# Optimization experiments

Hardware: AMD Instinct MI355X
Metric: run time of the kernel (lower is better)

Reference implementation:

```python
import jax, jax.numpy as jnp
import numpy as np

EPS = 1e-8


def setup_inputs() -> dict:
    key = jax.random.key(0)
    k1, k2, k3 = jax.random.split(key, 3)
    B, N, K, D = 64, 4096, 64, 256
    x = jax.random.normal(k1, (B, N, D), dtype=jnp.float32)
    mu = jax.random.normal(k2, (K, D), dtype=jnp.float32)
    log_sigma = jax.random.normal(k3, (K, D), dtype=jnp.float32) * 0.1
    return {"x": x, "mu": mu, "log_sigma": log_sigma, "n_slots": 8}


def reference(x, mu, log_sigma, n_slots):
    # cosine similarity: normalize then contract (avoids [B,N,K,D] broadcast)
    xn = x / jnp.maximum(jnp.linalg.norm(x, axis=-1, keepdims=True), EPS)
    mn = mu / jnp.maximum(jnp.linalg.norm(mu, axis=-1, keepdims=True), EPS)
    cos = jnp.einsum('bnd,kd->bnk', xn, mn)            # [B, N, K]
    cos_soft = jax.nn.softmax(cos, axis=-1)            # softmax over concepts
    r = jax.nn.softmax(cos_soft.sum(axis=1), axis=-1)  # [B, K]
    _, idx = jax.lax.top_k(r, n_slots)                 # [B, n_slots]
    mu_sample = mu[idx]                                # [B, n_slots, D]
    sigma_sample = jnp.exp(log_sigma[idx])             # [B, n_slots, D]
    noise = jax.random.normal(jax.random.key(42), mu_sample.shape, dtype=mu_sample.dtype)
    return mu_sample + sigma_sample * noise
```

## Files before the change

### kernel.cpp

```cpp
#include <hip/hip_runtime.h>
#include <math.h>
#include <stdint.h>

#define B_ 64
#define N_ 4096
#define K_ 64
#define D_ 256
#define NS_ 8
#define XPAD 260

#define FENCE_LGKM() asm volatile("s_waitcnt lgkmcnt(0)" ::: "memory")
#define CBAR() asm volatile("" ::: "memory")

__device__ __forceinline__ float fadd(float a, float b) { return __fadd_rn(a, b); }
__device__ __forceinline__ float fmul(float a, float b) { return __fmul_rn(a, b); }

__device__ __forceinline__ float np_expf(float x) {
  const float LOG2E = 1.442695040888963407359924681001892137f;
  float qf = rintf(__fmul_rn(x, LOG2E));
  float r = __fmaf_rn(qf, -6.93145752e-1f, x);
  r = __fmaf_rn(qf, -1.42860677e-6f, r);
  float num = __fmaf_rn(r, 5.082762527590693718096e-04f, 6.757896990527504603057e-03f);
  num = __fmaf_rn(num, r, 5.114512081637298353406e-02f);
  num = __fmaf_rn(num, r, 2.473615434895520810817e-01f);
  num = __fmaf_rn(num, r, 7.257664613233124478488e-01f);
  num = __fmaf_rn(num, r, 9.999999999980870924916e-01f);
  float den = __fmaf_rn(r, 2.159509375685829852307e-02f, -2.742335390411667452936e-01f);
  den = __fmaf_rn(den, r, 1.000000000000000000000e+00f);
  float poly = __fdiv_rn(num, den);
  int qi = (int)qf;
  float scale = __int_as_float((127 + qi) << 23);
  return __fmul_rn(poly, scale);
}

__device__ __forceinline__ uint32_t rotl32(uint32_t x, int r) {
  return (x << r) | (x >> (32 - r));
}
__device__ __forceinline__ float jax_normal_from_index(uint32_t i) {
  uint32_t x0 = 0u, x1 = i;
  const uint32_t ks0 = 0u, ks1 = 42u, ks2 = 0x1BD11BDAu ^ 0u ^ 42u;
  x0 += ks0; x1 += ks1;
#define TF_ROUND(r) { x0 += x1; x1 = rotl32(x1, (r)); x1 ^= x0; }
  TF_ROUND(13) TF_ROUND(15) TF_ROUND(26) TF_ROUND(6)
  x0 += ks1; x1 += ks2 + 1u;
  TF_ROUND(17) TF_ROUND(29) TF_ROUND(16) TF_ROUND(24)
  x0 += ks2; x1 += ks0 + 2u;
  TF_ROUND(13) TF_ROUND(15) TF_ROUND(26) TF_ROUND(6)
  x0 += ks0; x1 += ks1 + 3u;
  TF_ROUND(17) TF_ROUND(29) TF_ROUND(16) TF_ROUND(24)
  x0 += ks1; x1 += ks2 + 4u;
  TF_ROUND(13) TF_ROUND(15) TF_ROUND(26) TF_ROUND(6)
  x0 += ks2; x1 += ks0 + 5u;
#undef TF_ROUND
  uint32_t bits = x0 ^ x1;
  uint32_t fb = (bits >> 9) | 0x3f800000u;
  float f = __uint_as_float(fb) - 1.0f;
  const float lo = __uint_as_float(0xBF7FFFFFu);
  float u = f * 2.0f + lo;
  u = fmaxf(lo, u);
  float w = -log1pf(-u * u);
  float p;
  if (w < 5.0f) {
    w = w - 2.5f;
    p = 2.81022636e-08f;
    p = fmaf(p, w, 3.43273939e-07f);
    p = fmaf(p, w, -3.5233877e-06f);
    p = fmaf(p, w, -4.39150654e-06f);
    p = fmaf(p, w, 0.00021858087f);
    p = fmaf(p, w, -0.00125372503f);
    p = fmaf(p, w, -0.00417768164f);
    p = fmaf(p, w, 0.246640727f);
    p = fmaf(p, w, 1.50140941f);
  } else {
    w = sqrtf(w) - 3.0f;
    p = -0.000200214257f;
    p = fmaf(p, w, 0.000100950558f);
    p = fmaf(p, w, 0.00134934322f);
    p = fmaf(p, w, -0.00367342844f);
    p = fmaf(p, w, 0.00573950773f);
    p = fmaf(p, w, -0.0076224613f);
    p = fmaf(p, w, 0.00943887047f);
    p = fmaf(p, w, 1.00167406f);
    p = fmaf(p, w, 2.83297682f);
  }
  return 1.41421356f * (p * u);
}

__device__ __forceinline__ float np_pw128_sq(const float* p) {
  float t16[16];
#pragma unroll
  for (int L = 0; L < 16; ++L) {
    float q0 = p[L];       q0 = fmul(q0, q0);
    float q1 = p[L + 16];  q1 = fmul(q1, q1);
    float q2 = p[L + 32];  q2 = fmul(q2, q2);
    float q3 = p[L + 48];  q3 = fmul(q3, q3);
    float q4 = p[L + 64];  q4 = fmul(q4, q4);
    float q5 = p[L + 80];  q5 = fmul(q5, q5);
    float q6 = p[L + 96];  q6 = fmul(q6, q6);
    float q7 = p[L + 112]; q7 = fmul(q7, q7);
    t16[L] = fadd(fadd(fadd(q0, q4), fadd(q1, q5)), fadd(fadd(q2, q6), fadd(q3, q7)));
  }
  float u8[8];
#pragma unroll
  for (int L = 0; L < 8; ++L) u8[L] = fadd(t16[L], t16[L + 8]);
  float v4[4];
#pragma unroll
  for (int L = 0; L < 4; ++L) v4[L] = fadd(u8[L], u8[L + 4]);
  return fadd(fadd(v4[0], v4[2]), fadd(v4[1], v4[3]));
}

__device__ __forceinline__ float np_sum64(const float* a) {
  float t16[16];
#pragma unroll
  for (int L = 0; L < 16; ++L)
    t16[L] = fadd(fadd(a[L], a[16 + L]), fadd(a[32 + L], a[48 + L]));
  float u8[8];
#pragma unroll
  for (int L = 0; L < 8; ++L) u8[L] = fadd(t16[L], t16[L + 8]);
  float v4[4];
#pragma unroll
  for (int L = 0; L < 4; ++L) v4[L] = fadd(u8[L], u8[L + 4]);
  return fadd(fadd(v4[0], v4[2]), fadd(v4[1], v4[3]));
}

__global__ __launch_bounds__(64)
void prep_mnT(const float* __restrict__ mu, float4* __restrict__ mnT4) {
  const int k = threadIdx.x;
  const float* mrow = mu + k * D_;
  const float n2 = fadd(np_pw128_sq(mrow), np_pw128_sq(mrow + 128));
  const float den = fmaxf(__fsqrt_rn(n2), 1e-8f);
#pragma unroll 8
  for (int t = 0; t < 64; ++t) {
    float4 m = *(const float4*)&mrow[4 * t];
    float4 o;
    o.x = __fdiv_rn(m.x, den); o.y = __fdiv_rn(m.y, den);
    o.z = __fdiv_rn(m.z, den); o.w = __fdiv_rn(m.w, den);
    mnT4[t * K_ + k] = o;
  }
}

__global__ __launch_bounds__(1024, 1)
void xn_cos_softmax(const float* __restrict__ x,
                    const float4* __restrict__ mnT4_g,
                    float* __restrict__ p_ws) {
  __shared__ float4 mnT4[64][64];
  __shared__ float xst[16][4][XPAD];

  const int b = blockIdx.x;
  const int seg = blockIdx.y;
  const int tid = threadIdx.x;
  const int w = tid >> 6;
  const int lane = tid & 63;

#pragma unroll
  for (int i = 0; i < 4; ++i)
    ((float4*)mnT4)[tid * 4 + i] = mnT4_g[tid * 4 + i];
  __syncthreads();

  const int L16 = lane & 15;
  const int rowg = lane >> 4;

  float4 xr[4];
  {
    const int n0 = seg * 512 + w * 4;
#pragma unroll
    for (int r = 0; r < 4; ++r)
      xr[r] = *(const float4*)&x[(((size_t)b << 12) + n0 + r) * D_ + lane * 4];
  }

  for (int pass = 0; pass < 8; ++pass) {
    const int n0 = seg * 512 + pass * 64 + w * 4;

#pragma unroll
    for (int r = 0; r < 4; ++r)
      *(float4*)&xst[w][r][lane * 4] = xr[r];
    FENCE_LGKM();

    if (pass < 7) {
      const int n1 = n0 + 64;
#pragma unroll
      for (int r = 0; r < 4; ++r)
        xr[r] = *(const float4*)&x[(((size_t)b << 12) + n1 + r) * D_ + lane * 4];
    }

    float den4[4];
    {
      const float* rowp = &xst[w][rowg][0];
      float res2[2];
#pragma unroll
      for (int half = 0; half < 2; ++half) {
        const float* p = rowp + half * 128 + L16;
        float q0 = p[0];   q0 = fmul(q0, q0);
        float q1 = p[16];  q1 = fmul(q1, q1);
        float q2 = p[32];  q2 = fmul(q2, q2);
        float q3 = p[48];  q3 = fmul(q3, q3);
        float q4 = p[64];  q4 = fmul(q4, q4);
        float q5 = p[80];  q5 = fmul(q5, q5);
        float q6 = p[96];  q6 = fmul(q6, q6);
        float q7 = p[112]; q7 = fmul(q7, q7);
        const float t = fadd(fadd(fadd(q0, q4), fadd(q1, q5)),
                             fadd(fadd(q2, q6), fadd(q3, q7)));
        float u  = fadd(t, __shfl_xor(t, 8));
        float v  = fadd(u, __shfl_xor(u, 4));
        float w2 = fadd(v, __shfl_xor(v, 2));
        res2[half] = fadd(w2, __shfl_xor(w2, 1));
      }
      const float n2 = fadd(res2[0], res2[1]);
      const float den = fmaxf(__fsqrt_rn(n2), 1e-8f);
#pragma unroll
      for (int r = 0; r < 4; ++r) den4[r] = __shfl(den, 16 * r);
    }
    CBAR();

#pragma unroll
    for (int r = 0; r < 4; ++r) {
      float4 v = *(float4*)&xst[w][r][lane * 4];
      v.x = __fdiv_rn(v.x, den4[r]); v.y = __fdiv_rn(v.y, den4[r]);
      v.z = __fdiv_rn(v.z, den4[r]); v.w = __fdiv_rn(v.w, den4[r]);
      *(float4*)&xst[w][r][lane * 4] = v;
    }
    FENCE_LGKM();

    float acc[4][4];
#pragma unroll
    for (int r = 0; r < 4; ++r)
#pragma unroll
      for (int j = 0; j < 4; ++j) acc[r][j] = 0.f;

#pragma unroll 4
    for (int t = 0; t < 64; ++t) {
      const float4 m4 = mnT4[t][lane];
#pragma unroll
      for (int r = 0; r < 4; ++r) {
        const float4 x4 = *(const float4*)&xst[w][r][4 * t];
        acc[r][0] = fadd(acc[r][0], fmul(x4.x, m4.x));
        acc[r][1] = fadd(acc[r][1], fmul(x4.y, m4.y));
        acc[r][2] = fadd(acc[r][2], fmul(x4.z, m4.z));
        acc[r][3] = fadd(acc[r][3], fmul(x4.w, m4.w));
      }
    }

#pragma unroll
    for (int r = 0; r < 4; ++r) {
      const float cosr = fadd(fadd(acc[r][0], acc[r][1]), fadd(acc[r][2], acc[r][3]));
      float mx = cosr;
      mx = fmaxf(mx, __shfl_xor(mx, 1));
      mx = fmaxf(mx, __shfl_xor(mx, 2));
      mx = fmaxf(mx, __shfl_xor(mx, 4));
      mx = fmaxf(mx, __shfl_xor(mx, 8));
      mx = fmaxf(mx, __shfl_xor(mx, 16));
      mx = fmaxf(mx, __shfl_xor(mx, 32));
      const float e = np_expf(__fsub_rn(cosr, mx));
      float g1 = fadd(e, __shfl_xor(e, 16));
      float g2 = fadd(g1, __shfl_xor(g1, 32));
      float u  = fadd(g2, __shfl_xor(g2, 8));
      float v  = fadd(u, __shfl_xor(u, 4));
      float w2 = fadd(v, __shfl_xor(v, 2));
      float sres = fadd(w2, __shfl_xor(w2, 1));
      const float denom = __shfl(sres, 0);
      const float p = __fdiv_rn(e, denom);
      p_ws[(((size_t)b << 12) + n0 + r) * K_ + lane] = p;
    }
    CBAR();
  }
}

__global__ __launch_bounds__(256)
void pairwise_sum_n(const float* __restrict__ p_ws, float* __restrict__ s_part) {
  __shared__ float part[4][K_];
  const int b = blockIdx.x;
  const int g = blockIdx.y;
  const int w = threadIdx.x >> 6;
  const int k = threadIdx.x & 63;
  const float* base = p_ws + ((size_t)b << 12) * K_ + k;

  float l[2];
#pragma unroll 1
  for (int i = 0; i < 2; ++i) {
    const float* leaf = base + (size_t)(g * 8 + w * 2 + i) * 128 * K_;
    float c[16];
#pragma unroll
    for (int L = 0; L < 16; ++L) {
      const float* pL = leaf + (size_t)L * K_;
      const float q0 = pL[0 * 16 * K_];
      const float q1 = pL[1 * 16 * K_];
      const float q2 = pL[2 * 16 * K_];
      const float q3 = pL[3 * 16 * K_];
      const float q4 = pL[4 * 16 * K_];
      const float q5 = pL[5 * 16 * K_];
      const float q6 = pL[6 * 16 * K_];
      const float q7 = pL[7 * 16 * K_];
      c[L] = fadd(fadd(fadd(q0, q4), fadd(q1, q5)), fadd(fadd(q2, q6), fadd(q3, q7)));
    }
    float u8[8];
#pragma unroll
    for (int L = 0; L < 8; ++L) u8[L] = fadd(c[L], c[L + 8]);
    float v4[4];
#pragma unroll
    for (int L = 0; L < 4; ++L) v4[L] = fadd(u8[L], u8[L + 4]);
    l[i] = fadd(fadd(v4[0], v4[2]), fadd(v4[1], v4[3]));
  }
  part[w][k] = fadd(l[0], l[1]);
  __syncthreads();
  if (w == 0) {
    const float Sg = fadd(fadd(part[0][k], part[1][k]), fadd(part[2][k], part[3][k]));
    s_part[(b * 4 + g) * K_ + k] = Sg;
  }
}

__global__ __launch_bounds__(256)
void topk_sample(const float* __restrict__ s_part,
                 const float* __restrict__ mu,
                 const float* __restrict__ ls,
                 float* __restrict__ out) {
  __shared__ float sv[K_];
  __shared__ int sidx[NS_];
  const int b = blockIdx.x;
  const int t = threadIdx.x;
  if (t < K_) {
    const float S0 = s_part[(b * 4 + 0) * K_ + t];
    const float S1 = s_part[(b * 4 + 1) * K_ + t];
    const float S2 = s_part[(b * 4 + 2) * K_ + t];
    const float S3 = s_part[(b * 4 + 3) * K_ + t];
    sv[t] = fadd(fadd(S0, S1), fadd(S2, S3));
  }
  __syncthreads();
  if (t == 0) {
    float mx = sv[0];
    for (int k = 1; k < K_; ++k) mx = fmaxf(mx, sv[k]);
    float e[K_];
    for (int k = 0; k < K_; ++k) e[k] = np_expf(__fsub_rn(sv[k], mx));
    const float denom = np_sum64(e);
    float rv[K_];
    for (int k = 0; k < K_; ++k) rv[k] = __fdiv_rn(e[k], denom);
    for (int q = 0; q < NS_; ++q) {
      float best = -1.0e30f; int bi = 0;
      for (int k = 0; k < K_; ++k) {
        if (rv[k] > best) { best = rv[k]; bi = k; }
      }
      sidx[q] = bi;
      rv[bi] = -1.0e30f;
    }
  }
  __syncthreads();

  const int q = t >> 5;
  const int d0 = (t & 31) * 8;
  const int k = sidx[q];
  const float* mrow = mu + k * D_ + d0;
  const float* lrow = ls + k * D_ + d0;
  float* orow = out + ((size_t)b * NS_ + q) * D_ + d0;
  const uint32_t ibase = (uint32_t)(((b * NS_) + q) * D_ + d0);
#pragma unroll
  for (int j = 0; j < 8; ++j) {
    const float z = jax_normal_from_index(ibase + (uint32_t)j);
    orow[j] = fmaf(expf(lrow[j]), z, mrow[j]);
  }
}

extern "C" void kernel_launch(void* const* d_in, const int* in_sizes, int n_in,
                              void* d_out, int out_size, void* d_ws, size_t ws_size,
                              hipStream_t stream) {
  const float* x  = (const float*)d_in[0];
  const float* mu = (const float*)d_in[1];
  const float* ls = (const float*)d_in[2];
  float* out = (float*)d_out;
  (void)ws_size; (void)in_sizes; (void)n_in; (void)out_size;

  float*  p_ws   = (float*)d_ws;
  float*  s_part = (float*)((char*)d_ws + (size_t)67108864);
  float4* mnT4   = (float4*)((char*)d_ws + (size_t)67174400);

  prep_mnT<<<1, 64, 0, stream>>>(mu, mnT4);
  dim3 grid(B_, 8);
  xn_cos_softmax<<<grid, 1024, 0, stream>>>(x, mnT4, p_ws);
  dim3 grid2(B_, 4);
  pairwise_sum_n<<<grid2, 256, 0, stream>>>(p_ws, s_part);
  topk_sample<<<B_, 256, 0, stream>>>(s_part, mu, ls, out);
}
```

Measured before the change: 312.4 us.

## Software-pipeline softmax of previous pass into current dot-product loop

Splits the per-pass softmax (shuffle reductions, exp, divide, store) into stages spread across the 16 chunks of the next pass's dot-product loop, so shuffle latency overlaps with FMA/LDS work. The first pass writes its dummy softmax to a scratch buffer and a final epilogue stores the last pass. It also changes the LDS row padding from 260 to 264 floats. This raises register pressure (two 4x4 accumulator sets) and fully unrolls the dot loop.

```diff
diff --git a/kernel.cpp b/kernel.cpp
--- a/kernel.cpp
+++ b/kernel.cpp
@@ -7,7 +7,7 @@
 #define K_ 64
 #define D_ 256
 #define NS_ 8
-#define XPAD 260
+#define XPAD 264
 
 #define FENCE_LGKM() asm volatile("s_waitcnt lgkmcnt(0)" ::: "memory")
 #define CBAR() asm volatile("" ::: "memory")
@@ -139,10 +139,114 @@
   }
 }
 
+__device__ __forceinline__ void dot_pass_prev(
+    const float* __restrict__ xstw,
+    const float4 (* __restrict__ mnT4)[64],
+    int lane,
+    float (&acc)[4][4],
+    const float (&accP)[4][4],
+    float* __restrict__ pPrev)
+{
+  float cosP[4], mP[4], tP[4], eP[4], gP[4], denomP[4];
+#pragma unroll
+  for (int tc = 0; tc < 16; ++tc) {
+#pragma unroll
+    for (int tt = 0; tt < 4; ++tt) {
+      const int t = tc * 4 + tt;
+      const float4 m4 = mnT4[t][lane];
+#pragma unroll
+      for (int r = 0; r < 4; ++r) {
+        const float4 x4 = *(const float4*)&xstw[r * XPAD + 4 * t];
+        acc[r][0] = fadd(acc[r][0], fmul(x4.x, m4.x));
+        acc[r][1] = fadd(acc[r][1], fmul(x4.y, m4.y));
+        acc[r][2] = fadd(acc[r][2], fmul(x4.z, m4.z));
+        acc[r][3] = fadd(acc[r][3], fmul(x4.w, m4.w));
+      }
+    }
+    if (tc == 0) {
+#pragma unroll
+      for (int r = 0; r < 4; ++r) {
+        cosP[r] = fadd(fadd(accP[r][0], accP[r][1]), fadd(accP[r][2], accP[r][3]));
+        mP[r] = cosP[r];
+        tP[r] = __shfl_xor(mP[r], 1);
+      }
+    } else if (tc == 1) {
+#pragma unroll
+      for (int r = 0; r < 4; ++r) { mP[r] = fmaxf(mP[r], tP[r]); tP[r] = __shfl_xor(mP[r], 2); }
+    } else if (tc == 2) {
+#pragma unroll
+      for (int r = 0; r < 4; ++r) { mP[r] = fmaxf(mP[r], tP[r]); tP[r] = __shfl_xor(mP[r], 4); }
+    } else if (tc == 3) {
+#pragma unroll
+      for (int r = 0; r < 4; ++r) { mP[r] = fmaxf(mP[r], tP[r]); tP[r] = __shfl_xor(mP[r], 8); }
+    } else if (tc == 4) {
+#pragma unroll
+      for (int r = 0; r < 4; ++r) { mP[r] = fmaxf(mP[r], tP[r]); tP[r] = __shfl_xor(mP[r], 16); }
+    } else if (tc == 5) {
+#pragma unroll
+      for (int r = 0; r < 4; ++r) { mP[r] = fmaxf(mP[r], tP[r]); tP[r] = __shfl_xor(mP[r], 32); }
+    } else if (tc == 6) {
+#pragma unroll
+      for (int r = 0; r < 4; ++r) {
+        mP[r] = fmaxf(mP[r], tP[r]);
+        eP[r] = np_expf(__fsub_rn(cosP[r], mP[r]));
+      }
+    } else if (tc == 7) {
+#pragma unroll
+      for (int r = 0; r < 4; ++r) tP[r] = __shfl_xor(eP[r], 16);
+    } else if (tc == 8) {
+#pragma unroll
+      for (int r = 0; r < 4; ++r) { gP[r] = fadd(eP[r], tP[r]); tP[r] = __shfl_xor(gP[r], 32); }
+    } else if (tc == 9) {
+#pragma unroll
+      for (int r = 0; r < 4; ++r) { gP[r] = fadd(gP[r], tP[r]); tP[r] = __shfl_xor(gP[r], 8); }
+    } else if (tc == 10) {
+#pragma unroll
+      for (int r = 0; r < 4; ++r) { gP[r] = fadd(gP[r], tP[r]); tP[r] = __shfl_xor(gP[r], 4); }
+    } else if (tc == 11) {
+#pragma unroll
+      for (int r = 0; r < 4; ++r) { gP[r] = fadd(gP[r], tP[r]); tP[r] = __shfl_xor(gP[r], 2); }
+    } else if (tc == 12) {
+#pragma unroll
+      for (int r = 0; r < 4; ++r) { gP[r] = fadd(gP[r], tP[r]); tP[r] = __shfl_xor(gP[r], 1); }
+    } else if (tc == 13) {
+#pragma unroll
+      for (int r = 0; r < 4; ++r) { gP[r] = fadd(gP[r], tP[r]); denomP[r] = __shfl(gP[r], 0); }
+    } else if (tc == 14) {
+#pragma unroll
+      for (int r = 0; r < 4; ++r) pPrev[r * K_] = __fdiv_rn(eP[r], denomP[r]);
+    }
+  }
+}
+
+__device__ __forceinline__ void softmax_store(const float (&accP)[4][4], float* pdst) {
+#pragma unroll
+  for (int r = 0; r < 4; ++r) {
+    const float cosr = fadd(fadd(accP[r][0], accP[r][1]), fadd(accP[r][2], accP[r][3]));
+    float mx = cosr;
+    mx = fmaxf(mx, __shfl_xor(mx, 1));
+    mx = fmaxf(mx, __shfl_xor(mx, 2));
+    mx = fmaxf(mx, __shfl_xor(mx, 4));
+    mx = fmaxf(mx, __shfl_xor(mx, 8));
+    mx = fmaxf(mx, __shfl_xor(mx, 16));
+    mx = fmaxf(mx, __shfl_xor(mx, 32));
+    const float e = np_expf(__fsub_rn(cosr, mx));
+    float g1 = fadd(e, __shfl_xor(e, 16));
+    float g2 = fadd(g1, __shfl_xor(g1, 32));
+    float u  = fadd(g2, __shfl_xor(g2, 8));
+    float v  = fadd(u, __shfl_xor(u, 4));
+    float w2 = fadd(v, __shfl_xor(v, 2));
+    float sres = fadd(w2, __shfl_xor(w2, 1));
+    const float denom = __shfl(sres, 0);
+    pdst[r * K_] = __fdiv_rn(e, denom);
+  }
+}
+
 __global__ __launch_bounds__(1024, 1)
 void xn_cos_softmax(const float* __restrict__ x,
                     const float4* __restrict__ mnT4_g,
-                    float* __restrict__ p_ws) {
+                    float* __restrict__ p_ws,
+                    float* __restrict__ scr) {
   __shared__ float4 mnT4[64][64];
   __shared__ float xst[16][4][XPAD];
 
@@ -167,6 +271,13 @@
     for (int r = 0; r < 4; ++r)
       xr[r] = *(const float4*)&x[(((size_t)b << 12) + n0 + r) * D_ + lane * 4];
   }
+
+  float acc[4][4], accP[4][4];
+#pragma unroll
+  for (int r = 0; r < 4; ++r)
+#pragma unroll
+    for (int j = 0; j < 4; ++j) accP[r][j] = 0.f;
+  float* pPrev = scr + lane;
 
   for (int pass = 0; pass < 8; ++pass) {
     const int n0 = seg * 512 + pass * 64 + w * 4;
@@ -221,48 +332,23 @@
     }
     FENCE_LGKM();
 
-    float acc[4][4];
 #pragma unroll
     for (int r = 0; r < 4; ++r)
 #pragma unroll
       for (int j = 0; j < 4; ++j) acc[r][j] = 0.f;
 
-#pragma unroll 4
-    for (int t = 0; t < 64; ++t) {
-      const float4 m4 = mnT4[t][lane];
-#pragma unroll
-      for (int r = 0; r < 4; ++r) {
-        const float4 x4 = *(const float4*)&xst[w][r][4 * t];
-        acc[r][0] = fadd(acc[r][0], fmul(x4.x, m4.x));
-        acc[r][1] = fadd(acc[r][1], fmul(x4.y, m4.y));
-        acc[r][2] = fadd(acc[r][2], fmul(x4.z, m4.z));
-        acc[r][3] = fadd(acc[r][3], fmul(x4.w, m4.w));
-      }
-    }
-
-#pragma unroll
-    for (int r = 0; r < 4; ++r) {
-      const float cosr = fadd(fadd(acc[r][0], acc[r][1]), fadd(acc[r][2], acc[r][3]));
-      float mx = cosr;
-      mx = fmaxf(mx, __shfl_xor(mx, 1));
-      mx = fmaxf(mx, __shfl_xor(mx, 2));
-      mx = fmaxf(mx, __shfl_xor(mx, 4));
-      mx = fmaxf(mx, __shfl_xor(mx, 8));
-      mx = fmaxf(mx, __shfl_xor(mx, 16));
-      mx = fmaxf(mx, __shfl_xor(mx, 32));
-      const float e = np_expf(__fsub_rn(cosr, mx));
-      float g1 = fadd(e, __shfl_xor(e, 16));
-      float g2 = fadd(g1, __shfl_xor(g1, 32));
-      float u  = fadd(g2, __shfl_xor(g2, 8));
-      float v  = fadd(u, __shfl_xor(u, 4));
-      float w2 = fadd(v, __shfl_xor(v, 2));
-      float sres = fadd(w2, __shfl_xor(w2, 1));
-      const float denom = __shfl(sres, 0);
-      const float p = __fdiv_rn(e, denom);
-      p_ws[(((size_t)b << 12) + n0 + r) * K_ + lane] = p;
-    }
+    dot_pass_prev(&xst[w][0][0], mnT4, lane, acc, accP, pPrev);
+
+#pragma unroll
+    for (int r = 0; r < 4; ++r)
+#pragma unroll
+      for (int j = 0; j < 4; ++j) accP[r][j] = acc[r][j];
+    pPrev = p_ws + (((size_t)b << 12) + n0) * K_ + lane;
+
     CBAR();
   }
+
+  softmax_store(accP, pPrev);
 }
 
 __global__ __launch_bounds__(256)
@@ -370,10 +456,11 @@
   float*  p_ws   = (float*)d_ws;
   float*  s_part = (float*)((char*)d_ws + (size_t)67108864);
   float4* mnT4   = (float4*)((char*)d_ws + (size_t)67174400);
+  float*  scr    = (float*)((char*)d_ws + (size_t)67239936);
 
   prep_mnT<<<1, 64, 0, stream>>>(mu, mnT4);
   dim3 grid(B_, 8);
-  xn_cos_softmax<<<grid, 1024, 0, stream>>>(x, mnT4, p_ws);
+  xn_cos_softmax<<<grid, 1024, 0, stream>>>(x, mnT4, p_ws, scr);
   dim3 grid2(B_, 4);
   pairwise_sum_n<<<grid2, 256, 0, stream>>>(p_ws, s_part);
   topk_sample<<<B_, 256, 0, stream>>>(s_part, mu, ls, out);
```

After: 304.8 us, median of 2. 2.4% less time.

## Split normalization and cosine-softmax into separate kernels via materialized xn

Applied to the files above, without the earlier changes.

Splits the fused normalize+cosine+softmax kernel into two kernels. The first writes the normalized x to a workspace buffer. The second computes cosines with 8 rows per wave and higher occupancy, reading xn straight from global memory instead of staging it in LDS. The aim is to free LDS and registers so more blocks run per CU, at the cost of an extra 256 MB write and read of xn. The workspace size decides at runtime which path runs, and the old fused kernel stays as the fallback.

```diff
diff --git a/kernel.cpp b/kernel.cpp
--- a/kernel.cpp
+++ b/kernel.cpp
@@ -7,7 +7,7 @@
 #define K_ 64
 #define D_ 256
 #define NS_ 8
-#define XPAD 260
+#define XPAD 264
 
 #define FENCE_LGKM() asm volatile("s_waitcnt lgkmcnt(0)" ::: "memory")
 #define CBAR() asm volatile("" ::: "memory")
@@ -139,18 +139,161 @@
   }
 }
 
-__global__ __launch_bounds__(1024, 1)
-void xn_cos_softmax(const float* __restrict__ x,
-                    const float4* __restrict__ mnT4_g,
-                    float* __restrict__ p_ws) {
-  __shared__ float4 mnT4[64][64];
+__device__ __forceinline__ void np_norm4(const float* rowp, int L16, float* den_out) {
+  float res2[2];
+#pragma unroll
+  for (int half = 0; half < 2; ++half) {
+    const float* p = rowp + half * 128 + L16;
+    float q0 = p[0];   q0 = fmul(q0, q0);
+    float q1 = p[16];  q1 = fmul(q1, q1);
+    float q2 = p[32];  q2 = fmul(q2, q2);
+    float q3 = p[48];  q3 = fmul(q3, q3);
+    float q4 = p[64];  q4 = fmul(q4, q4);
+    float q5 = p[80];  q5 = fmul(q5, q5);
+    float q6 = p[96];  q6 = fmul(q6, q6);
+    float q7 = p[112]; q7 = fmul(q7, q7);
+    const float t = fadd(fadd(fadd(q0, q4), fadd(q1, q5)),
+                         fadd(fadd(q2, q6), fadd(q3, q7)));
+    float u  = fadd(t, __shfl_xor(t, 8));
+    float v  = fadd(u, __shfl_xor(u, 4));
+    float w2 = fadd(v, __shfl_xor(v, 2));
+    res2[half] = fadd(w2, __shfl_xor(w2, 1));
+  }
+  const float n2 = fadd(res2[0], res2[1]);
+  *den_out = fmaxf(__fsqrt_rn(n2), 1e-8f);
+}
+
+__device__ __forceinline__ float np_softmax64(float cosr) {
+  float mx = cosr;
+  mx = fmaxf(mx, __shfl_xor(mx, 1));
+  mx = fmaxf(mx, __shfl_xor(mx, 2));
+  mx = fmaxf(mx, __shfl_xor(mx, 4));
+  mx = fmaxf(mx, __shfl_xor(mx, 8));
+  mx = fmaxf(mx, __shfl_xor(mx, 16));
+  mx = fmaxf(mx, __shfl_xor(mx, 32));
+  const float e = np_expf(__fsub_rn(cosr, mx));
+  float g1 = fadd(e, __shfl_xor(e, 16));
+  float g2 = fadd(g1, __shfl_xor(g1, 32));
+  float u  = fadd(g2, __shfl_xor(g2, 8));
+  float v  = fadd(u, __shfl_xor(u, 4));
+  float w2 = fadd(v, __shfl_xor(v, 2));
+  float sres = fadd(w2, __shfl_xor(w2, 1));
+  const float denom = __shfl(sres, 0);
+  return __fdiv_rn(e, denom);
+}
+
+__global__ __launch_bounds__(1024, 8)
+void xn_write(const float* __restrict__ x, float* __restrict__ xn) {
   __shared__ float xst[16][4][XPAD];
-
   const int b = blockIdx.x;
   const int seg = blockIdx.y;
   const int tid = threadIdx.x;
   const int w = tid >> 6;
   const int lane = tid & 63;
+  const int L16 = lane & 15;
+  const int rowg = lane >> 4;
+
+  float4 xr[4];
+  {
+    const int n0 = seg * 512 + w * 4;
+#pragma unroll
+    for (int r = 0; r < 4; ++r)
+      xr[r] = *(const float4*)&x[(((size_t)b << 12) + n0 + r) * D_ + lane * 4];
+  }
+
+  for (int pass = 0; pass < 8; ++pass) {
+    const int n0 = seg * 512 + pass * 64 + w * 4;
+#pragma unroll
+    for (int r = 0; r < 4; ++r)
+      *(float4*)&xst[w][r][lane * 4] = xr[r];
+    FENCE_LGKM();
+
+    if (pass < 7) {
+      const int n1 = n0 + 64;
+#pragma unroll
+      for (int r = 0; r < 4; ++r)
+        xr[r] = *(const float4*)&x[(((size_t)b << 12) + n1 + r) * D_ + lane * 4];
+    }
+
+    float den4[4];
+    {
+      float den;
+      np_norm4(&xst[w][rowg][0], L16, &den);
+#pragma unroll
+      for (int r = 0; r < 4; ++r) den4[r] = __shfl(den, 16 * r);
+    }
+
+#pragma unroll
+    for (int r = 0; r < 4; ++r) {
+      const float4 v = *(const float4*)&xst[w][r][lane * 4];
+      float4 o;
+      o.x = __fdiv_rn(v.x, den4[r]); o.y = __fdiv_rn(v.y, den4[r]);
+      o.z = __fdiv_rn(v.z, den4[r]); o.w = __fdiv_rn(v.w, den4[r]);
+      *(float4*)&xn[(((size_t)b << 12) + n0 + r) * D_ + lane * 4] = o;
+    }
+    CBAR();
+  }
+}
+
+__global__ __launch_bounds__(512, 4)
+void cos_softmax_xn(const float* __restrict__ xn,
+                    const float4* __restrict__ mnT4_g,
+                    float* __restrict__ p_ws) {
+  __shared__ float4 mnT4[64][64];
+  const int b = blockIdx.x;
+  const int seg = blockIdx.y;
+  const int tid = threadIdx.x;
+  const int w = tid >> 6;
+  const int lane = tid & 63;
+
+#pragma unroll
+  for (int i = 0; i < 8; ++i)
+    ((float4*)mnT4)[tid * 8 + i] = mnT4_g[tid * 8 + i];
+  __syncthreads();
+
+  for (int pass = 0; pass < 4; ++pass) {
+    const int rowbase = seg * 256 + pass * 64 + w * 8;
+    const float* xrow = xn + (((size_t)b << 12) + rowbase) * D_;
+
+    float acc[8][4];
+#pragma unroll
+    for (int r = 0; r < 8; ++r)
+#pragma unroll
+      for (int j = 0; j < 4; ++j) acc[r][j] = 0.f;
+
+#pragma unroll 4
+    for (int t = 0; t < 64; ++t) {
+      const float4 m4 = mnT4[t][lane];
+#pragma unroll
+      for (int r = 0; r < 8; ++r) {
+        const float4 x4 = *(const float4*)&xrow[(size_t)r * D_ + 4 * t];
+        acc[r][0] = fadd(acc[r][0], fmul(x4.x, m4.x));
+        acc[r][1] = fadd(acc[r][1], fmul(x4.y, m4.y));
+        acc[r][2] = fadd(acc[r][2], fmul(x4.z, m4.z));
+        acc[r][3] = fadd(acc[r][3], fmul(x4.w, m4.w));
+      }
+    }
+
+#pragma unroll
+    for (int r = 0; r < 8; ++r) {
+      const float cosr = fadd(fadd(acc[r][0], acc[r][1]), fadd(acc[r][2], acc[r][3]));
+      const float p = np_softmax64(cosr);
+      p_ws[(((size_t)b << 12) + rowbase + r) * K_ + lane] = p;
+    }
+  }
+}
+
+__global__ __launch_bounds__(1024, 1)
+void xn_cos_softmax_legacy(const float* __restrict__ x,
+                           const float4* __restrict__ mnT4_g,
+                           float* __restrict__ p_ws) {
+  __shared__ float4 mnT4[64][64];
+  __shared__ float xst[16][4][XPAD];
+  const int b = blockIdx.x;
+  const int seg = blockIdx.y;
+  const int tid = threadIdx.x;
+  const int w = tid >> 6;
+  const int lane = tid & 63;
 
 #pragma unroll
   for (int i = 0; i < 4; ++i)
@@ -170,7 +313,6 @@
 
   for (int pass = 0; pass < 8; ++pass) {
     const int n0 = seg * 512 + pass * 64 + w * 4;
-
 #pragma unroll
     for (int r = 0; r < 4; ++r)
       *(float4*)&xst[w][r][lane * 4] = xr[r];
@@ -185,28 +327,8 @@
 
     float den4[4];
     {
-      const float* rowp = &xst[w][rowg][0];
-      float res2[2];
-#pragma unroll
-      for (int half = 0; half < 2; ++half) {
-        const float* p = rowp + half * 128 + L16;
-        float q0 = p[0];   q0 = fmul(q0, q0);
-        float q1 = p[16];  q1 = fmul(q1, q1);
-        float q2 = p[32];  q2 = fmul(q2, q2);
-        float q3 = p[48];  q3 = fmul(q3, q3);
-        float q4 = p[64];  q4 = fmul(q4, q4);
-        float q5 = p[80];  q5 = fmul(q5, q5);
-        float q6 = p[96];  q6 = fmul(q6, q6);
-        float q7 = p[112]; q7 = fmul(q7, q7);
-        const float t = fadd(fadd(fadd(q0, q4), fadd(q1, q5)),
-                             fadd(fadd(q2, q6), fadd(q3, q7)));
-        float u  = fadd(t, __shfl_xor(t, 8));
-        float v  = fadd(u, __shfl_xor(u, 4));
-        float w2 = fadd(v, __shfl_xor(v, 2));
-        res2[half] = fadd(w2, __shfl_xor(w2, 1));
-      }
-      const float n2 = fadd(res2[0], res2[1]);
-      const float den = fmaxf(__fsqrt_rn(n2), 1e-8f);
+      float den;
+      np_norm4(&xst[w][rowg][0], L16, &den);
 #pragma unroll
       for (int r = 0; r < 4; ++r) den4[r] = __shfl(den, 16 * r);
     }
@@ -243,22 +365,7 @@
 #pragma unroll
     for (int r = 0; r < 4; ++r) {
       const float cosr = fadd(fadd(acc[r][0], acc[r][1]), fadd(acc[r][2], acc[r][3]));
-      float mx = cosr;
-      mx = fmaxf(mx, __shfl_xor(mx, 1));
-      mx = fmaxf(mx, __shfl_xor(mx, 2));
-      mx = fmaxf(mx, __shfl_xor(mx, 4));
-      mx = fmaxf(mx, __shfl_xor(mx, 8));
-      mx = fmaxf(mx, __shfl_xor(mx, 16));
-      mx = fmaxf(mx, __shfl_xor(mx, 32));
-      const float e = np_expf(__fsub_rn(cosr, mx));
-      float g1 = fadd(e, __shfl_xor(e, 16));
-      float g2 = fadd(g1, __shfl_xor(g1, 32));
-      float u  = fadd(g2, __shfl_xor(g2, 8));
-      float v  = fadd(u, __shfl_xor(u, 4));
-      float w2 = fadd(v, __shfl_xor(v, 2));
-      float sres = fadd(w2, __shfl_xor(w2, 1));
-      const float denom = __shfl(sres, 0);
-      const float p = __fdiv_rn(e, denom);
+      const float p = np_softmax64(cosr);
       p_ws[(((size_t)b << 12) + n0 + r) * K_ + lane] = p;
     }
     CBAR();
@@ -365,16 +472,36 @@
   const float* mu = (const float*)d_in[1];
   const float* ls = (const float*)d_in[2];
   float* out = (float*)d_out;
-  (void)ws_size; (void)in_sizes; (void)n_in; (void)out_size;
-
-  float*  p_ws   = (float*)d_ws;
-  float*  s_part = (float*)((char*)d_ws + (size_t)67108864);
-  float4* mnT4   = (float4*)((char*)d_ws + (size_t)67174400);
-
-  prep_mnT<<<1, 64, 0, stream>>>(mu, mnT4);
-  dim3 grid(B_, 8);
-  xn_cos_softmax<<<grid, 1024, 0, stream>>>(x, mnT4, p_ws);
-  dim3 grid2(B_, 4);
-  pairwise_sum_n<<<grid2, 256, 0, stream>>>(p_ws, s_part);
-  topk_sample<<<B_, 256, 0, stream>>>(s_part, mu, ls, out);
-}
+  (void)in_sizes; (void)n_in; (void)out_size;
+
+  const size_t XN_BYTES = (size_t)B_ * N_ * D_ * 4;
+  const size_t P_BYTES  = (size_t)B_ * N_ * K_ * 4;
+  const size_t NEED_T1  = XN_BYTES + P_BYTES + 65536 + 65536;
+
+  if (ws_size >= NEED_T1) {
+    float*  xn     = (float*)d_ws;
+    float*  p_ws   = (float*)((char*)d_ws + XN_BYTES);
+    float*  s_part = (float*)((char*)d_ws + XN_BYTES + P_BYTES);
+    float4* mnT4   = (float4*)((char*)d_ws + XN_BYTES + P_BYTES + 65536);
+
+    prep_mnT<<<1, 64, 0, stream>>>(mu, mnT4);
+    dim3 gridA(B_, 8);
+    xn_write<<<gridA, 1024, 0, stream>>>(x, xn);
+    dim3 gridB(B_, 16);
+    cos_softmax_xn<<<gridB, 512, 0, stream>>>(xn, mnT4, p_ws);
+    dim3 grid2(B_, 4);
+    pairwise_sum_n<<<grid2, 256, 0, stream>>>(p_ws, s_part);
+    topk_sample<<<B_, 256, 0, stream>>>(s_part, mu, ls, out);
+  } else {
+    float*  p_ws   = (float*)d_ws;
+    float*  s_part = (float*)((char*)d_ws + P_BYTES);
+    float4* mnT4   = (float4*)((char*)d_ws + P_BYTES + 65536);
+
+    prep_mnT<<<1, 64, 0, stream>>>(mu, mnT4);
+    dim3 grid(B_, 8);
+    xn_cos_softmax_legacy<<<grid, 1024, 0, stream>>>(x, mnT4, p_ws);
+    dim3 grid2(B_, 4);
+    pairwise_sum_n<<<grid2, 256, 0, stream>>>(p_ws, s_part);
+    topk_sample<<<B_, 256, 0, stream>>>(s_part, mu, ls, out);
+  }
+}
```

Measured after the change: 1.115 ms. +257.0%, slower.

## Broadcast normalized x via readlane instead of LDS reloads in cosine matmul

Applied to the files above, without the earlier changes.

Normalizes x in registers from the prefetched global values instead of writing the normalized rows back to LDS. The inner dot-product loop now broadcasts x elements to the wave with readlane (scalar registers) rather than reading float4 from LDS, and that loop is fully unrolled. The x staging pad also changes. This is meant to remove LDS traffic and waits in the hot loop, at the cost of many readlane instructions and higher register pressure from full unrolling.

```diff
diff --git a/kernel.cpp b/kernel.cpp
--- a/kernel.cpp
+++ b/kernel.cpp
@@ -7,13 +7,17 @@
 #define K_ 64
 #define D_ 256
 #define NS_ 8
-#define XPAD 260
+#define XPAD 264
 
 #define FENCE_LGKM() asm volatile("s_waitcnt lgkmcnt(0)" ::: "memory")
 #define CBAR() asm volatile("" ::: "memory")
 
 __device__ __forceinline__ float fadd(float a, float b) { return __fadd_rn(a, b); }
 __device__ __forceinline__ float fmul(float a, float b) { return __fmul_rn(a, b); }
+
+__device__ __forceinline__ float rdlane(float v, int lane) {
+  return __int_as_float(__builtin_amdgcn_readlane(__float_as_int(v), lane));
+}
 
 __device__ __forceinline__ float np_expf(float x) {
   const float LOG2E = 1.442695040888963407359924681001892137f;
@@ -139,6 +143,49 @@
   }
 }
 
+__device__ __forceinline__ void np_norm4(const float* rowp, int L16, float* den_out) {
+  float res2[2];
+#pragma unroll
+  for (int half = 0; half < 2; ++half) {
+    const float* p = rowp + half * 128 + L16;
+    float q0 = p[0];   q0 = fmul(q0, q0);
+    float q1 = p[16];  q1 = fmul(q1, q1);
+    float q2 = p[32];  q2 = fmul(q2, q2);
+    float q3 = p[48];  q3 = fmul(q3, q3);
+    float q4 = p[64];  q4 = fmul(q4, q4);
+    float q5 = p[80];  q5 = fmul(q5, q5);
+    float q6 = p[96];  q6 = fmul(q6, q6);
+    float q7 = p[112]; q7 = fmul(q7, q7);
+    const float t = fadd(fadd(fadd(q0, q4), fadd(q1, q5)),
+                         fadd(fadd(q2, q6), fadd(q3, q7)));
+    float u  = fadd(t, __shfl_xor(t, 8));
+    float v  = fadd(u, __shfl_xor(u, 4));
+    float w2 = fadd(v, __shfl_xor(v, 2));
+    res2[half] = fadd(w2, __shfl_xor(w2, 1));
+  }
+  const float n2 = fadd(res2[0], res2[1]);
+  *den_out = fmaxf(__fsqrt_rn(n2), 1e-8f);
+}
+
+__device__ __forceinline__ float np_softmax64(float cosr) {
+  float mx = cosr;
+  mx = fmaxf(mx, __shfl_xor(mx, 1));
+  mx = fmaxf(mx, __shfl_xor(mx, 2));
+  mx = fmaxf(mx, __shfl_xor(mx, 4));
+  mx = fmaxf(mx, __shfl_xor(mx, 8));
+  mx = fmaxf(mx, __shfl_xor(mx, 16));
+  mx = fmaxf(mx, __shfl_xor(mx, 32));
+  const float e = np_expf(__fsub_rn(cosr, mx));
+  float g1 = fadd(e, __shfl_xor(e, 16));
+  float g2 = fadd(g1, __shfl_xor(g1, 32));
+  float u  = fadd(g2, __shfl_xor(g2, 8));
+  float v  = fadd(u, __shfl_xor(u, 4));
+  float w2 = fadd(v, __shfl_xor(v, 2));
+  float sres = fadd(w2, __shfl_xor(w2, 1));
+  const float denom = __shfl(sres, 0);
+  return __fdiv_rn(e, denom);
+}
+
 __global__ __launch_bounds__(1024, 1)
 void xn_cos_softmax(const float* __restrict__ x,
                     const float4* __restrict__ mnT4_g,
@@ -176,6 +223,24 @@
       *(float4*)&xst[w][r][lane * 4] = xr[r];
     FENCE_LGKM();
 
+    float den4[4];
+    {
+      float den;
+      np_norm4(&xst[w][rowg][0], L16, &den);
+#pragma unroll
+      for (int r = 0; r < 4; ++r) den4[r] = __shfl(den, 16 * r);
+    }
+    CBAR();
+
+    float4 xnr[4];
+#pragma unroll
+    for (int r = 0; r < 4; ++r) {
+      xnr[r].x = __fdiv_rn(xr[r].x, den4[r]);
+      xnr[r].y = __fdiv_rn(xr[r].y, den4[r]);
+      xnr[r].z = __fdiv_rn(xr[r].z, den4[r]);
+      xnr[r].w = __fdiv_rn(xr[r].w, den4[r]);
+    }
+
     if (pass < 7) {
       const int n1 = n0 + 64;
 #pragma unroll
@@ -183,85 +248,34 @@
         xr[r] = *(const float4*)&x[(((size_t)b << 12) + n1 + r) * D_ + lane * 4];
     }
 
-    float den4[4];
-    {
-      const float* rowp = &xst[w][rowg][0];
-      float res2[2];
-#pragma unroll
-      for (int half = 0; half < 2; ++half) {
-        const float* p = rowp + half * 128 + L16;
-        float q0 = p[0];   q0 = fmul(q0, q0);
-        float q1 = p[16];  q1 = fmul(q1, q1);
-        float q2 = p[32];  q2 = fmul(q2, q2);
-        float q3 = p[48];  q3 = fmul(q3, q3);
-        float q4 = p[64];  q4 = fmul(q4, q4);
-        float q5 = p[80];  q5 = fmul(q5, q5);
-        float q6 = p[96];  q6 = fmul(q6, q6);
-        float q7 = p[112]; q7 = fmul(q7, q7);
-        const float t = fadd(fadd(fadd(q0, q4), fadd(q1, q5)),
-                             fadd(fadd(q2, q6), fadd(q3, q7)));
-        float u  = fadd(t, __shfl_xor(t, 8));
-        float v  = fadd(u, __shfl_xor(u, 4));
-        float w2 = fadd(v, __shfl_xor(v, 2));
-        res2[half] = fadd(w2, __shfl_xor(w2, 1));
-      }
-      const float n2 = fadd(res2[0], res2[1]);
-      const float den = fmaxf(__fsqrt_rn(n2), 1e-8f);
-#pragma unroll
-      for (int r = 0; r < 4; ++r) den4[r] = __shfl(den, 16 * r);
-    }
-    CBAR();
-
-#pragma unroll
-    for (int r = 0; r < 4; ++r) {
-      float4 v = *(float4*)&xst[w][r][lane * 4];
-      v.x = __fdiv_rn(v.x, den4[r]); v.y = __fdiv_rn(v.y, den4[r]);
-      v.z = __fdiv_rn(v.z, den4[r]); v.w = __fdiv_rn(v.w, den4[r]);
-      *(float4*)&xst[w][r][lane * 4] = v;
-    }
-    FENCE_LGKM();
-
     float acc[4][4];
 #pragma unroll
     for (int r = 0; r < 4; ++r)
 #pragma unroll
       for (int j = 0; j < 4; ++j) acc[r][j] = 0.f;
 
-#pragma unroll 4
+#pragma unroll
     for (int t = 0; t < 64; ++t) {
       const float4 m4 = mnT4[t][lane];
 #pragma unroll
       for (int r = 0; r < 4; ++r) {
-        const float4 x4 = *(const float4*)&xst[w][r][4 * t];
-        acc[r][0] = fadd(acc[r][0], fmul(x4.x, m4.x));
-        acc[r][1] = fadd(acc[r][1], fmul(x4.y, m4.y));
-        acc[r][2] = fadd(acc[r][2], fmul(x4.z, m4.z));
-        acc[r][3] = fadd(acc[r][3], fmul(x4.w, m4.w));
+        const float x0 = rdlane(xnr[r].x, t);
+        const float x1 = rdlane(xnr[r].y, t);
+        const float x2 = rdlane(xnr[r].z, t);
+        const float x3 = rdlane(xnr[r].w, t);
+        acc[r][0] = fadd(acc[r][0], fmul(x0, m4.x));
+        acc[r][1] = fadd(acc[r][1], fmul(x1, m4.y));
+        acc[r][2] = fadd(acc[r][2], fmul(x2, m4.z));
+        acc[r][3] = fadd(acc[r][3], fmul(x3, m4.w));
       }
     }
 
 #pragma unroll
     for (int r = 0; r < 4; ++r) {
       const float cosr = fadd(fadd(acc[r][0], acc[r][1]), fadd(acc[r][2], acc[r][3]));
-      float mx = cosr;
-      mx = fmaxf(mx, __shfl_xor(mx, 1));
-      mx = fmaxf(mx, __shfl_xor(mx, 2));
-      mx = fmaxf(mx, __shfl_xor(mx, 4));
-      mx = fmaxf(mx, __shfl_xor(mx, 8));
-      mx = fmaxf(mx, __shfl_xor(mx, 16));
-      mx = fmaxf(mx, __shfl_xor(mx, 32));
-      const float e = np_expf(__fsub_rn(cosr, mx));
-      float g1 = fadd(e, __shfl_xor(e, 16));
-      float g2 = fadd(g1, __shfl_xor(g1, 32));
-      float u  = fadd(g2, __shfl_xor(g2, 8));
-      float v  = fadd(u, __shfl_xor(u, 4));
-      float w2 = fadd(v, __shfl_xor(v, 2));
-      float sres = fadd(w2, __shfl_xor(w2, 1));
-      const float denom = __shfl(sres, 0);
-      const float p = __fdiv_rn(e, denom);
+      const float p = np_softmax64(cosr);
       p_ws[(((size_t)b << 12) + n0 + r) * K_ + lane] = p;
     }
-    CBAR();
   }
 }
 
```

After: 349.7 us. 11.9% more time.
